# Kernel optimization log

Measured on AMD Instinct MI355X. Metric: run time of the kernel, lower is better.

Reference implementation:

```python
import jax, jax.numpy as jnp
import numpy as np

F = 16          # features
C = 128         # context features
H = 256         # conditioner hidden
L = 8           # coupling layers
K = 8           # spline bins
TB = 3.0        # tail bound
T = F // 2      # transform features per layer (8)
PDIM = 3 * K - 1  # params per transformed feature (23), tails='linear'
MIN_W = MIN_H = MIN_D = 1e-3
B = 65536


def _feature_split(layer):
    ev = np.arange(0, F, 2)
    od = np.arange(1, F, 2)
    tr, idn = (ev, od) if layer % 2 == 0 else (od, ev)  # mask>0 => transform
    inv = np.argsort(np.concatenate([idn, tr]))
    return idn, tr, inv


def _rq_spline(x, uw, uh, ud):
    """Monotonic rational-quadratic spline with linear tails (nflows semantics).
    x: [B,T]; uw/uh: [B,T,K]; ud: [B,T,K-1]. Returns (y, logabsdet) per element."""
    const = np.log(np.expm1(1.0 - MIN_D))  # pad value so boundary derivative == 1
    ud = jnp.pad(ud, ((0, 0), (0, 0), (1, 1)), constant_values=const)  # [B,T,K+1]
    inside = (x >= -TB) & (x <= TB)
    xs = jnp.clip(x, -TB, TB)

    w = jax.nn.softmax(uw, axis=-1)
    w = MIN_W + (1.0 - MIN_W * K) * w
    cw = jnp.pad(jnp.cumsum(w, -1), ((0, 0), (0, 0), (1, 0)))
    cw = 2.0 * TB * cw - TB
    cw = cw.at[..., 0].set(-TB).at[..., -1].set(TB)
    w = cw[..., 1:] - cw[..., :-1]

    d = MIN_D + jax.nn.softplus(ud)  # [B,T,K+1]

    h = jax.nn.softmax(uh, axis=-1)
    h = MIN_H + (1.0 - MIN_H * K) * h
    ch = jnp.pad(jnp.cumsum(h, -1), ((0, 0), (0, 0), (1, 0)))
    ch = 2.0 * TB * ch - TB
    ch = ch.at[..., 0].set(-TB).at[..., -1].set(TB)
    h = ch[..., 1:] - ch[..., :-1]

    # bin search on cumulative widths (forward direction)
    idx = jnp.clip(jnp.sum((xs[..., None] >= cw).astype(jnp.int32), -1) - 1, 0, K - 1)
    g = lambda a: jnp.take_along_axis(a, idx[..., None], axis=-1)[..., 0]

    x0, bw = g(cw[..., :K]), g(w)
    y0, bh = g(ch[..., :K]), g(h)
    delta = g(h / w)
    d0, d1 = g(d[..., :K]), g(d[..., 1:])

    th = (xs - x0) / bw
    th1m = th * (1.0 - th)
    num = bh * (delta * th * th + d0 * th1m)
    den = delta + (d0 + d1 - 2.0 * delta) * th1m
    y = y0 + num / den
    dnum = delta * delta * (d1 * th * th + 2.0 * delta * th1m + d0 * (1.0 - th) ** 2)
    ld = jnp.log(dnum) - 2.0 * jnp.log(den)
    return jnp.where(inside, y, x), jnp.where(inside, ld, 0.0)


def setup_inputs() -> dict:
    key = jax.random.key(0)
    ks = jax.random.split(key, 8)
    inputs = jax.random.normal(ks[0], (B, F), jnp.float32)
    context = jax.random.normal(ks[1], (B, C), jnp.float32)
    s = lambda k, shape, fan: jax.random.normal(k, shape, jnp.float32) / np.sqrt(fan)
    W1 = s(ks[2], (L, T + C, H), T + C)
    b1 = jnp.zeros((L, H), jnp.float32)
    W2 = s(ks[3], (L, H, H), H)
    b2 = jnp.zeros((L, H), jnp.float32)
    W3 = s(ks[4], (L, H, T * PDIM), H)
    b3 = jnp.zeros((L, T * PDIM), jnp.float32)
    rng = np.random.default_rng(0)  # fixed-at-init RandomPermutation buffers
    perms = jnp.asarray(np.stack([rng.permutation(F) for _ in range(L - 1)]), jnp.int32)
    return dict(inputs=inputs, context=context, W1=W1, b1=b1, W2=W2, b2=b2,
                W3=W3, b3=b3, perms=perms)


def reference(inputs, context, W1, b1, W2, b2, W3, b3, perms):
    x = jnp.clip(inputs, -1.0, 1.0)
    logdet = jnp.zeros(x.shape[0], x.dtype)
    for i in range(L):
        idn, tr, inv = _feature_split(i)
        xi = x[:, idn]
        xt = x[:, tr]
        hdn = jax.nn.relu(jnp.concatenate([xi, context], -1) @ W1[i] + b1[i])
        hdn = jax.nn.relu(hdn @ W2[i] + b2[i])
        p = (hdn @ W3[i] + b3[i]).reshape(-1, T, PDIM)
        yt, ld = _rq_spline(xt, p[..., :K], p[..., K:2 * K], p[..., 2 * K:])
        x = jnp.concatenate([xi, yt], -1)[:, inv]
        logdet = logdet + jnp.sum(ld, -1)
        if i < L - 1:
            x = x[:, perms[i]]
    return jnp.clip(x, -1.0, 1.0), logdet
```

## Files before the change

### kernel.cpp

```cpp
#include <hip/hip_runtime.h>
#include <math.h>

#define BATCH 65536
#define FDIM 16
#define CDIM 128
#define HDIM 256
#define NL 8
#define KBINS 8
#define TDIM 8
#define PD 23
#define TBV 3.0f
#define K1 160
#define N3 184
#define N3P 192
#define PSTR 197
#define MR 64
#define XSTR 40

typedef _Float16 f16;
typedef __attribute__((ext_vector_type(8))) _Float16 f16x8;
typedef __attribute__((ext_vector_type(4))) float f32x4;

__global__ __launch_bounds__(256)
void conv_w1_kernel(const float* __restrict__ W1,
                    f16* __restrict__ Wh, f16* __restrict__ Wl) {
    int idx = blockIdx.x * 256 + threadIdx.x;
    if (idx >= NL * HDIM * K1) return;
    int l = idx / (HDIM * K1);
    int rem = idx - l * (HDIM * K1);
    int n = rem / K1;
    int k = rem - n * K1;
    int row = (k < 128) ? (8 + k) : ((k < 136) ? (k - 128) : -1);
    float v = (row >= 0) ? W1[((size_t)l * 136 + row) * HDIM + n] : 0.f;
    f16 hv = (f16)v;
    Wh[idx] = hv; Wl[idx] = (f16)(v - (float)hv);
}

__global__ __launch_bounds__(256)
void conv_w2_kernel(const float* __restrict__ W2,
                    f16* __restrict__ Wh, f16* __restrict__ Wl) {
    int idx = blockIdx.x * 256 + threadIdx.x;
    if (idx >= NL * HDIM * HDIM) return;
    int l = idx / (HDIM * HDIM);
    int rem = idx - l * (HDIM * HDIM);
    int n = rem >> 8;
    int k = rem & 255;
    float v = W2[((size_t)l * HDIM + k) * HDIM + n];
    f16 hv = (f16)v;
    Wh[idx] = hv; Wl[idx] = (f16)(v - (float)hv);
}

__global__ __launch_bounds__(256)
void conv_w3_kernel(const float* __restrict__ W3,
                    f16* __restrict__ Wh, f16* __restrict__ Wl) {
    int idx = blockIdx.x * 256 + threadIdx.x;
    if (idx >= NL * N3P * HDIM) return;
    int l = idx / (N3P * HDIM);
    int rem = idx - l * (N3P * HDIM);
    int n = rem >> 8;
    int k = rem & 255;
    float v = (n < N3) ? W3[((size_t)l * HDIM + k) * N3 + n] : 0.f;
    f16 hv = (f16)v;
    Wh[idx] = hv; Wl[idx] = (f16)(v - (float)hv);
}

__global__ __launch_bounds__(256)
void conv_ctx_kernel(const float* __restrict__ ctx,
                     f16* __restrict__ ch, f16* __restrict__ cl) {
    size_t idx = ((size_t)blockIdx.x * 256 + threadIdx.x) * 4;
    if (idx >= (size_t)BATCH * CDIM) return;
    float4 v = *(const float4*)&ctx[idx];
    f16 h;
    h = (f16)v.x; ch[idx + 0] = h; cl[idx + 0] = (f16)(v.x - (float)h);
    h = (f16)v.y; ch[idx + 1] = h; cl[idx + 1] = (f16)(v.y - (float)h);
    h = (f16)v.z; ch[idx + 2] = h; cl[idx + 2] = (f16)(v.z - (float)h);
    h = (f16)v.w; ch[idx + 3] = h; cl[idx + 3] = (f16)(v.w - (float)h);
}

__device__ __forceinline__ float softplusf(float v) {
    return fmaxf(v, 0.f) + log1pf(expf(-fabsf(v)));
}

__device__ __forceinline__ void gld16(const f16* src, f16* dst) {
    __builtin_amdgcn_global_load_lds(
        (const __attribute__((address_space(1))) unsigned int*)src,
        (__attribute__((address_space(3))) unsigned int*)dst, 16, 0, 0);
}

template<int N> __device__ __forceinline__ void vmw() {
    asm volatile("s_waitcnt vmcnt(%0)" :: "n"(N) : "memory");
}
__device__ __forceinline__ void lgkmw() {
    asm volatile("s_waitcnt lgkmcnt(0)" ::: "memory");
}
__device__ __forceinline__ void barr() {
    __builtin_amdgcn_s_barrier();
    __builtin_amdgcn_sched_barrier(0);
}
__device__ __forceinline__ void lgkm_bar() {
    asm volatile("s_waitcnt lgkmcnt(0)" ::: "memory");
    __builtin_amdgcn_s_barrier();
    __builtin_amdgcn_sched_barrier(0);
}

__global__ __launch_bounds__(512, 1)
void flow_kernel(const float* __restrict__ in,
                 const f16* __restrict__ ctxh, const f16* __restrict__ ctxl,
                 const f16* __restrict__ W1h, const f16* __restrict__ W1l,
                 const f16* __restrict__ W2h, const f16* __restrict__ W2l,
                 const f16* __restrict__ W3h, const f16* __restrict__ W3l,
                 const float* __restrict__ b1, const float* __restrict__ b2,
                 const float* __restrict__ b3, const int* __restrict__ perms,
                 float* __restrict__ out) {
    __shared__ __align__(16) f16 sCtx[16384];
    __shared__ __align__(16) char warena[65536];
    __shared__ __align__(16) f16 sH[16384];
    __shared__ __align__(16) f16 sXi[2][MR * XSTR];
    __shared__ float sX[2][MR][17];
    __shared__ float sY[MR][9];
    __shared__ float sLd[MR][9];
    __shared__ float sLdet[MR];
    __shared__ float sBias[768];
    __shared__ int   sPerm[(NL - 1) * FDIM];

    float* sP = (float*)warena;

    const int tid = threadIdx.x;
    const int lane = tid & 63;
    const int w = tid >> 6;
    const int lr = lane & 15, lh = lane >> 4;
    const int bid = blockIdx.x;
    const int wgid = (bid & 7) * 32 + (bid >> 3);
    const int wcol0 = w * 32;
    const int wc3 = (w < 4) ? w * 32 : 128 + (w - 4) * 16;

    char* const wbuf = warena + w * 8192;

    auto bRd = [&](int lc) -> int {
        return lc * 64 + (((lh + (lc >> 1)) & 3) << 4);
    };

    auto stageB = [&](const f16* Wh, const f16* Wl, int b, int kt, int KD,
                      int colBase, int NC) {
        char* dst = wbuf + b * 4096;
        #pragma unroll
        for (int ii = 0; ii < 2; ++ii) {
            if (ii * 16 < NC) {
                int si = ii * 64 + lane;
                int c = si >> 2, pos = si & 3;
                int seg = (pos - (c >> 1)) & 3;
                const f16* sh = Wh + (size_t)(colBase + c) * KD + kt * 32 + seg * 8;
                const f16* sl = Wl + (size_t)(colBase + c) * KD + kt * 32 + seg * 8;
                gld16(sh, (f16*)(dst + ii * 1024 + lane * 16));
                gld16(sl, (f16*)(dst + NC * 64 + ii * 1024 + lane * 16));
            }
        }
    };

    for (int rb = 0; rb < 4; ++rb) {
        const int rbase = (rb * 256 + wgid) * MR;
        lgkm_bar();

        {
            int r = tid >> 3, c2 = (tid & 7) * 2;
            float2 v = *(const float2*)&in[(size_t)(rbase + r) * FDIM + c2];
            sX[0][r][c2 + 0] = fminf(fmaxf(v.x, -1.f), 1.f);
            sX[0][r][c2 + 1] = fminf(fmaxf(v.y, -1.f), 1.f);
        }
        if (tid < MR) sLdet[tid] = 0.f;
        if (rb == 0 && tid < (NL - 1) * FDIM) sPerm[tid] = perms[tid];

        #pragma unroll
        for (int s = 0; s < 4; ++s) {
            int slot = s * 512 + tid;
            int p = slot >> 10, sp = slot & 1023;
            int row = sp >> 4, blk = sp & 15;
            const f16* src = (p ? ctxl : ctxh)
                           + (size_t)(rbase + row) * CDIM + (blk ^ (row & 7)) * 8;
            gld16(src, &sCtx[slot * 8]);
        }

        int cur = 0;
        for (int l = 0; l < NL; ++l) {
            lgkm_bar();

            {
                float bv1 = (tid < 256) ? b1[l * HDIM + tid]
                                        : b2[l * HDIM + (tid - 256)];
                float bv3 = b3[l * N3 + (tid < N3 ? tid : N3 - 1)];
                sBias[tid] = bv1;
                if (tid < N3) sBias[512 + tid] = bv3;
            }
            if (tid < MR) {
                int r = tid, off = 1 - (l & 1);
                #pragma unroll
                for (int k = 0; k < 8; ++k) {
                    float v = sX[cur][r][2 * k + off];
                    f16 hv = (f16)v;
                    sXi[0][r * XSTR + k] = hv;
                    sXi[1][r * XSTR + k] = (f16)(v - (float)hv);
                }
                #pragma unroll
                for (int k = 8; k < 32; ++k) {
                    sXi[0][r * XSTR + k] = (f16)0.f;
                    sXi[1][r * XSTR + k] = (f16)0.f;
                }
            }
            const f16* W1hL = W1h + (size_t)l * HDIM * K1;
            const f16* W1lL = W1l + (size_t)l * HDIM * K1;
            const f16* W2hL = W2h + (size_t)l * HDIM * HDIM;
            const f16* W2lL = W2l + (size_t)l * HDIM * HDIM;
            const f16* W3hL = W3h + (size_t)l * N3P * HDIM;
            const f16* W3lL = W3l + (size_t)l * N3P * HDIM;
            stageB(W1hL, W1lL, 0, 0, K1, wcol0, 32);
            stageB(W1hL, W1lL, 1, 1, K1, wcol0, 32);
            lgkm_bar();

            f32x4 acc[4][2];
            #pragma unroll
            for (int i = 0; i < 4; ++i)
                #pragma unroll
                for (int j = 0; j < 2; ++j) acc[i][j] = (f32x4){0.f, 0.f, 0.f, 0.f};
            #pragma unroll
            for (int kt = 0; kt < 5; ++kt) {
                if (kt < 4) vmw<4>(); else vmw<0>();
                f16x8 ah[4], al[4];
                if (kt < 4) {
                    #pragma unroll
                    for (int i = 0; i < 4; ++i) {
                        int row = i * 16 + lr;
                        int byo = row * 256 + ((kt * 64 + lh * 16) ^ ((row & 7) << 4));
                        ah[i] = *(const f16x8*)((const char*)sCtx + byo);
                        al[i] = *(const f16x8*)((const char*)sCtx + 16384 + byo);
                    }
                } else {
                    #pragma unroll
                    for (int i = 0; i < 4; ++i) {
                        int row = i * 16 + lr;
                        ah[i] = *(const f16x8*)&sXi[0][row * XSTR + lh * 8];
                        al[i] = *(const f16x8*)&sXi[1][row * XSTR + lh * 8];
                    }
                }
                const char* bb = wbuf + (kt & 1) * 4096;
                __builtin_amdgcn_s_setprio(1);
                #pragma unroll
                for (int j = 0; j < 2; ++j) {
                    int cb = bRd(j * 16 + lr);
                    f16x8 bh = *(const f16x8*)(bb + cb);
                    f16x8 bl = *(const f16x8*)(bb + 2048 + cb);
                    #pragma unroll
                    for (int i = 0; i < 4; ++i) {
                        acc[i][j] = __builtin_amdgcn_mfma_f32_16x16x32_f16(ah[i], bh, acc[i][j], 0, 0, 0);
                        acc[i][j] = __builtin_amdgcn_mfma_f32_16x16x32_f16(ah[i], bl, acc[i][j], 0, 0, 0);
                        acc[i][j] = __builtin_amdgcn_mfma_f32_16x16x32_f16(al[i], bh, acc[i][j], 0, 0, 0);
                    }
                }
                __builtin_amdgcn_s_setprio(0);
                if (kt + 2 < 5) {
                    lgkmw();
                    stageB(W1hL, W1lL, kt & 1, kt + 2, K1, wcol0, 32);
                }
            }
            #pragma unroll
            for (int j = 0; j < 2; ++j) {
                int col = wcol0 + j * 16 + lr;
                float bv = sBias[col];
                #pragma unroll
                for (int i = 0; i < 4; ++i)
                    #pragma unroll
                    for (int q = 0; q < 4; ++q) {
                        float v = fmaxf(acc[i][j][q] + bv, 0.f);
                        int row = i * 16 + lh * 4 + q;
                        int e = ((row << 8) + col) ^ ((row & 7) << 3);
                        sH[e] = (f16)v;
                    }
            }
            stageB(W2hL, W2lL, 0, 0, HDIM, wcol0, 32);
            stageB(W2hL, W2lL, 1, 1, HDIM, wcol0, 32);
            lgkm_bar();

            #pragma unroll
            for (int i = 0; i < 4; ++i)
                #pragma unroll
                for (int j = 0; j < 2; ++j) acc[i][j] = (f32x4){0.f, 0.f, 0.f, 0.f};
            #pragma unroll
            for (int kt = 0; kt < 8; ++kt) {
                if (kt < 7) vmw<4>(); else vmw<0>();
                int k0 = kt * 32 + lh * 8;
                f16x8 ah[4];
                #pragma unroll
                for (int i = 0; i < 4; ++i) {
                    int row = i * 16 + lr;
                    int e = ((row << 8) + k0) ^ ((row & 7) << 3);
                    ah[i] = *(const f16x8*)&sH[e];
                }
                const char* bb = wbuf + (kt & 1) * 4096;
                __builtin_amdgcn_s_setprio(1);
                #pragma unroll
                for (int j = 0; j < 2; ++j) {
                    int cb = bRd(j * 16 + lr);
                    f16x8 bh = *(const f16x8*)(bb + cb);
                    f16x8 bl = *(const f16x8*)(bb + 2048 + cb);
                    #pragma unroll
                    for (int i = 0; i < 4; ++i) {
                        acc[i][j] = __builtin_amdgcn_mfma_f32_16x16x32_f16(ah[i], bh, acc[i][j], 0, 0, 0);
                        acc[i][j] = __builtin_amdgcn_mfma_f32_16x16x32_f16(ah[i], bl, acc[i][j], 0, 0, 0);
                    }
                }
                __builtin_amdgcn_s_setprio(0);
                if (kt + 2 < 8) {
                    lgkmw();
                    stageB(W2hL, W2lL, kt & 1, kt + 2, HDIM, wcol0, 32);
                }
            }
            barr();
            #pragma unroll
            for (int j = 0; j < 2; ++j) {
                int col = wcol0 + j * 16 + lr;
                float bv = sBias[256 + col];
                #pragma unroll
                for (int i = 0; i < 4; ++i)
                    #pragma unroll
                    for (int q = 0; q < 4; ++q) {
                        float v = fmaxf(acc[i][j][q] + bv, 0.f);
                        int row = i * 16 + lh * 4 + q;
                        int e = ((row << 8) + col) ^ ((row & 7) << 3);
                        sH[e] = (f16)v;
                    }
            }
            {
                const int NC3 = (w < 4) ? 32 : 16;
                stageB(W3hL, W3lL, 0, 0, HDIM, wc3, NC3);
                stageB(W3hL, W3lL, 1, 1, HDIM, wc3, NC3);
            }
            lgkm_bar();

            f32x4 acc3[4][2];
            #pragma unroll
            for (int i = 0; i < 4; ++i)
                #pragma unroll
                for (int j = 0; j < 2; ++j) acc3[i][j] = (f32x4){0.f, 0.f, 0.f, 0.f};
            {
                const int NC3 = (w < 4) ? 32 : 16;
                const int nc64 = NC3 * 64;
                #pragma unroll
                for (int kt = 0; kt < 8; ++kt) {
                    if (kt < 7) { if (w < 4) vmw<4>(); else vmw<2>(); }
                    else vmw<0>();
                    int k0 = kt * 32 + lh * 8;
                    f16x8 ah[4];
                    #pragma unroll
                    for (int i = 0; i < 4; ++i) {
                        int row = i * 16 + lr;
                        int e = ((row << 8) + k0) ^ ((row & 7) << 3);
                        ah[i] = *(const f16x8*)&sH[e];
                    }
                    const char* bb = wbuf + (kt & 1) * 4096;
                    __builtin_amdgcn_s_setprio(1);
                    {
                        int cb = bRd(lr);
                        f16x8 bh = *(const f16x8*)(bb + cb);
                        f16x8 bl = *(const f16x8*)(bb + nc64 + cb);
                        #pragma unroll
                        for (int i = 0; i < 4; ++i) {
                            acc3[i][0] = __builtin_amdgcn_mfma_f32_16x16x32_f16(ah[i], bh, acc3[i][0], 0, 0, 0);
                            acc3[i][0] = __builtin_amdgcn_mfma_f32_16x16x32_f16(ah[i], bl, acc3[i][0], 0, 0, 0);
                        }
                    }
                    if (w < 4) {
                        int cb = bRd(16 + lr);
                        f16x8 bh = *(const f16x8*)(bb + cb);
                        f16x8 bl = *(const f16x8*)(bb + nc64 + cb);
                        #pragma unroll
                        for (int i = 0; i < 4; ++i) {
                            acc3[i][1] = __builtin_amdgcn_mfma_f32_16x16x32_f16(ah[i], bh, acc3[i][1], 0, 0, 0);
                            acc3[i][1] = __builtin_amdgcn_mfma_f32_16x16x32_f16(ah[i], bl, acc3[i][1], 0, 0, 0);
                        }
                    }
                    __builtin_amdgcn_s_setprio(0);
                    if (kt + 2 < 8) {
                        lgkmw();
                        stageB(W3hL, W3lL, kt & 1, kt + 2, HDIM, wc3, NC3);
                    }
                }
            }
            barr();
            {
                int col = wc3 + lr;
                float bv = (col < N3) ? sBias[512 + col] : 0.f;
                #pragma unroll
                for (int i = 0; i < 4; ++i)
                    #pragma unroll
                    for (int q = 0; q < 4; ++q) {
                        int row = i * 16 + lh * 4 + q;
                        sP[row * PSTR + col] = acc3[i][0][q] + bv;
                    }
                if (w < 4) {
                    int col1 = wc3 + 16 + lr;
                    float bv1 = sBias[512 + col1];
                    #pragma unroll
                    for (int i = 0; i < 4; ++i)
                        #pragma unroll
                        for (int q = 0; q < 4; ++q) {
                            int row = i * 16 + lh * 4 + q;
                            sP[row * PSTR + col1] = acc3[i][1][q] + bv1;
                        }
                }
            }
            lgkm_bar();

            {
                int r = tid & 63, t = tid >> 6;
                float xin = sX[cur][r][2 * t + (l & 1)];
                const float* pp = &sP[r * PSTR + t * PD];
                bool inside = (xin >= -TBV) && (xin <= TBV);
                float xs = fminf(fmaxf(xin, -TBV), TBV);

                float e0, e1, e2, e3, e4, e5, e6, e7;
                {
                    float a0 = pp[0], a1 = pp[1], a2 = pp[2], a3 = pp[3];
                    float a4 = pp[4], a5 = pp[5], a6 = pp[6], a7 = pp[7];
                    float m = fmaxf(fmaxf(fmaxf(a0, a1), fmaxf(a2, a3)),
                                    fmaxf(fmaxf(a4, a5), fmaxf(a6, a7)));
                    e0 = expf(a0 - m); e1 = expf(a1 - m); e2 = expf(a2 - m); e3 = expf(a3 - m);
                    e4 = expf(a4 - m); e5 = expf(a5 - m); e6 = expf(a6 - m); e7 = expf(a7 - m);
                }
                float swv = ((e0 + e1) + (e2 + e3)) + ((e4 + e5) + (e6 + e7));
                float cwc = (1.f - 0.001f * KBINS) / swv;
                float x0 = -TBV, x1 = TBV;
                int idx = 0;
                bool done = false;
                {
                    float cs = 0.f;
                    float ee[7] = {e0, e1, e2, e3, e4, e5, e6};
                    #pragma unroll
                    for (int k = 0; k < 7; ++k) {
                        cs += 0.001f + cwc * ee[k];
                        float nxt = 2.f * TBV * cs - TBV;
                        bool ge = (xs >= nxt);
                        x0 = ge ? nxt : x0;
                        idx += ge ? 1 : 0;
                        x1 = (!ge && !done) ? nxt : x1;
                        done = done || !ge;
                    }
                }
                float y0 = -TBV, y1 = TBV;
                {
                    float a0 = pp[8], a1 = pp[9], a2 = pp[10], a3 = pp[11];
                    float a4 = pp[12], a5 = pp[13], a6 = pp[14], a7 = pp[15];
                    float m = fmaxf(fmaxf(fmaxf(a0, a1), fmaxf(a2, a3)),
                                    fmaxf(fmaxf(a4, a5), fmaxf(a6, a7)));
                    float f0 = expf(a0 - m), f1 = expf(a1 - m), f2 = expf(a2 - m), f3 = expf(a3 - m);
                    float f4 = expf(a4 - m), f5 = expf(a5 - m), f6 = expf(a6 - m), f7 = expf(a7 - m);
                    float shv = ((f0 + f1) + (f2 + f3)) + ((f4 + f5) + (f6 + f7));
                    float chc = (1.f - 0.001f * KBINS) / shv;
                    float cs = 0.f;
                    float ff[7] = {f0, f1, f2, f3, f4, f5, f6};
                    #pragma unroll
                    for (int k = 0; k < 7; ++k) {
                        cs += 0.001f + chc * ff[k];
                        float nxt = 2.f * TBV * cs - TBV;
                        y0 = (k < idx) ? nxt : y0;
                        y1 = (k == idx) ? nxt : y1;
                    }
                }
                float udm = pp[16 + (idx > 0 ? idx - 1 : 0)];
                float udp = pp[16 + (idx < 7 ? idx : 6)];
                float d0 = (idx > 0) ? 0.001f + softplusf(udm) : 1.f;
                float d1 = (idx < 7) ? 0.001f + softplusf(udp) : 1.f;

                float bw = x1 - x0, bh2 = y1 - y0;
                float delta = bh2 / bw;
                float th = (xs - x0) / bw;
                float th1m = th * (1.f - th);
                float num = bh2 * (delta * th * th + d0 * th1m);
                float den = delta + (d0 + d1 - 2.f * delta) * th1m;
                float y = y0 + num / den;
                float omth = 1.f - th;
                float dnum = delta * delta * (d1 * th * th + 2.f * delta * th1m + d0 * omth * omth);
                float ldv = logf(dnum) - 2.f * logf(den);
                sY[r][t] = inside ? y : xin;
                sLd[r][t] = inside ? ldv : 0.f;
            }
            lgkm_bar();

            {
                int r = tid >> 3, f0 = (tid & 7) * 2;
                if (l < NL - 1) {
                    #pragma unroll
                    for (int ff = 0; ff < 2; ++ff) {
                        int f = f0 + ff;
                        int g = sPerm[l * FDIM + f];
                        float v = ((g & 1) == (l & 1)) ? sY[r][g >> 1] : sX[cur][r][g];
                        sX[cur ^ 1][r][f] = v;
                    }
                    if (f0 == 0) {
                        float s = 0.f;
                        #pragma unroll
                        for (int t = 0; t < 8; ++t) s += sLd[r][t];
                        sLdet[r] += s;
                    }
                } else {
                    float ov[2];
                    #pragma unroll
                    for (int ff = 0; ff < 2; ++ff) {
                        int f = f0 + ff;
                        float v = ((f & 1) == (l & 1)) ? sY[r][f >> 1] : sX[cur][r][f];
                        ov[ff] = fminf(fmaxf(v, -1.f), 1.f);
                    }
                    float2 o = {ov[0], ov[1]};
                    *(float2*)&out[(size_t)(rbase + r) * FDIM + f0] = o;
                    if (f0 == 0) {
                        float s = 0.f;
                        #pragma unroll
                        for (int t = 0; t < 8; ++t) s += sLd[r][t];
                        out[(size_t)BATCH * FDIM + rbase + r] = sLdet[r] + s;
                    }
                }
            }
            cur ^= 1;
        }
    }
}

extern "C" void kernel_launch(void* const* d_in, const int* in_sizes, int n_in,
                              void* d_out, int out_size, void* d_ws, size_t ws_size,
                              hipStream_t stream) {
    (void)in_sizes; (void)n_in; (void)out_size; (void)ws_size;
    const float* inputs  = (const float*)d_in[0];
    const float* context = (const float*)d_in[1];
    const float* W1 = (const float*)d_in[2];
    const float* b1 = (const float*)d_in[3];
    const float* W2 = (const float*)d_in[4];
    const float* b2 = (const float*)d_in[5];
    const float* W3 = (const float*)d_in[6];
    const float* b3 = (const float*)d_in[7];
    const int*   perms = (const int*)d_in[8];
    float* out = (float*)d_out;

    f16* W1h = (f16*)d_ws;
    f16* W1l = W1h + (size_t)NL * HDIM * K1;
    f16* W2h = W1l + (size_t)NL * HDIM * K1;
    f16* W2l = W2h + (size_t)NL * HDIM * HDIM;
    f16* W3h = W2l + (size_t)NL * HDIM * HDIM;
    f16* W3l = W3h + (size_t)NL * N3P * HDIM;
    f16* ctxh = W3l + (size_t)NL * N3P * HDIM;
    f16* ctxl = ctxh + (size_t)BATCH * CDIM;

    int n1 = NL * HDIM * K1;
    conv_w1_kernel<<<(n1 + 255) / 256, 256, 0, stream>>>(W1, W1h, W1l);
    int n2 = NL * HDIM * HDIM;
    conv_w2_kernel<<<(n2 + 255) / 256, 256, 0, stream>>>(W2, W2h, W2l);
    int n3 = NL * N3P * HDIM;
    conv_w3_kernel<<<(n3 + 255) / 256, 256, 0, stream>>>(W3, W3h, W3l);
    int nc = BATCH * CDIM / 4;
    conv_ctx_kernel<<<(nc + 255) / 256, 256, 0, stream>>>(context, ctxh, ctxl);

    flow_kernel<<<256, 512, 0, stream>>>(
        inputs, ctxh, ctxl, W1h, W1l, W2h, W2l, W3h, W3l,
        b1, b2, b3, perms, out);
}
```

Measured before the change: 520.4 us.

## Split hidden activations into hi/lo f16 and keep W2/W3 single f16

Moves the fp16 hi/lo error-compensation split from the W2/W3 weights to the hidden activations. Weights are now converted to a single f16 copy, which halves weight staging traffic and the per-wave LDS weight buffers. The low part of each activation is stored in a new shared region carved out of the weight arena. The MFMA count stays the same, but W2/W3 weights lose their low-order correction, which may reduce accuracy. An extra barrier is added after layer 1, presumably because the activation low part now shares LDS with the weight staging buffers.

```diff
diff --git a/kernel.cpp b/kernel.cpp
--- a/kernel.cpp
+++ b/kernel.cpp
@@ -37,22 +37,18 @@
 }
 
 __global__ __launch_bounds__(256)
-void conv_w2_kernel(const float* __restrict__ W2,
-                    f16* __restrict__ Wh, f16* __restrict__ Wl) {
+void conv_w2_kernel(const float* __restrict__ W2, f16* __restrict__ Ws) {
     int idx = blockIdx.x * 256 + threadIdx.x;
     if (idx >= NL * HDIM * HDIM) return;
     int l = idx / (HDIM * HDIM);
     int rem = idx - l * (HDIM * HDIM);
     int n = rem >> 8;
     int k = rem & 255;
-    float v = W2[((size_t)l * HDIM + k) * HDIM + n];
-    f16 hv = (f16)v;
-    Wh[idx] = hv; Wl[idx] = (f16)(v - (float)hv);
+    Ws[idx] = (f16)W2[((size_t)l * HDIM + k) * HDIM + n];
 }
 
 __global__ __launch_bounds__(256)
-void conv_w3_kernel(const float* __restrict__ W3,
-                    f16* __restrict__ Wh, f16* __restrict__ Wl) {
+void conv_w3_kernel(const float* __restrict__ W3, f16* __restrict__ Ws) {
     int idx = blockIdx.x * 256 + threadIdx.x;
     if (idx >= NL * N3P * HDIM) return;
     int l = idx / (N3P * HDIM);
@@ -60,8 +56,7 @@
     int n = rem >> 8;
     int k = rem & 255;
     float v = (n < N3) ? W3[((size_t)l * HDIM + k) * N3 + n] : 0.f;
-    f16 hv = (f16)v;
-    Wh[idx] = hv; Wl[idx] = (f16)(v - (float)hv);
+    Ws[idx] = (f16)v;
 }
 
 __global__ __launch_bounds__(256)
@@ -107,8 +102,7 @@
 void flow_kernel(const float* __restrict__ in,
                  const f16* __restrict__ ctxh, const f16* __restrict__ ctxl,
                  const f16* __restrict__ W1h, const f16* __restrict__ W1l,
-                 const f16* __restrict__ W2h, const f16* __restrict__ W2l,
-                 const f16* __restrict__ W3h, const f16* __restrict__ W3l,
+                 const f16* __restrict__ W2s, const f16* __restrict__ W3s,
                  const float* __restrict__ b1, const float* __restrict__ b2,
                  const float* __restrict__ b3, const int* __restrict__ perms,
                  float* __restrict__ out) {
@@ -123,6 +117,7 @@
     __shared__ float sBias[768];
     __shared__ int   sPerm[(NL - 1) * FDIM];
 
+    f16* hLo = (f16*)(warena + 32768);
     float* sP = (float*)warena;
 
     const int tid = threadIdx.x;
@@ -134,28 +129,23 @@
     const int wcol0 = w * 32;
     const int wc3 = (w < 4) ? w * 32 : 128 + (w - 4) * 16;
 
-    char* const wbuf = warena + w * 8192;
-
     auto bRd = [&](int lc) -> int {
         return lc * 64 + (((lh + (lc >> 1)) & 3) << 4);
     };
 
-    auto stageB = [&](const f16* Wh, const f16* Wl, int b, int kt, int KD,
-                      int colBase, int NC) {
-        char* dst = wbuf + b * 4096;
+    auto stageB1 = [&](int b, int kt) {
+        char* dst = warena + w * 8192 + b * 4096;
+        const f16* WhL = W1h;
+        (void)WhL;
         #pragma unroll
         for (int ii = 0; ii < 2; ++ii) {
-            if (ii * 16 < NC) {
-                int si = ii * 64 + lane;
-                int c = si >> 2, pos = si & 3;
-                int seg = (pos - (c >> 1)) & 3;
-                const f16* sh = Wh + (size_t)(colBase + c) * KD + kt * 32 + seg * 8;
-                const f16* sl = Wl + (size_t)(colBase + c) * KD + kt * 32 + seg * 8;
-                gld16(sh, (f16*)(dst + ii * 1024 + lane * 16));
-                gld16(sl, (f16*)(dst + NC * 64 + ii * 1024 + lane * 16));
-            }
+            int si = ii * 64 + lane;
+            int c = si >> 2, pos = si & 3;
+            int seg = (pos - (c >> 1)) & 3;
+            (void)c; (void)seg; (void)dst; (void)kt;
         }
     };
+    (void)stageB1;
 
     for (int rb = 0; rb < 4; ++rb) {
         const int rbase = (rb * 256 + wgid) * MR;
@@ -202,18 +192,44 @@
                 }
                 #pragma unroll
                 for (int k = 8; k < 32; ++k) {
-                    sXi[0][r * XSTR + k] = (f16)0.f;
-                    sXi[1][r * XSTR + k] = (f16)0.f;
+                    sXi[0][tid * XSTR + k] = (f16)0.f;
+                    sXi[1][tid * XSTR + k] = (f16)0.f;
                 }
             }
             const f16* W1hL = W1h + (size_t)l * HDIM * K1;
             const f16* W1lL = W1l + (size_t)l * HDIM * K1;
-            const f16* W2hL = W2h + (size_t)l * HDIM * HDIM;
-            const f16* W2lL = W2l + (size_t)l * HDIM * HDIM;
-            const f16* W3hL = W3h + (size_t)l * N3P * HDIM;
-            const f16* W3lL = W3l + (size_t)l * N3P * HDIM;
-            stageB(W1hL, W1lL, 0, 0, K1, wcol0, 32);
-            stageB(W1hL, W1lL, 1, 1, K1, wcol0, 32);
+            const f16* W2L  = W2s + (size_t)l * HDIM * HDIM;
+            const f16* W3L  = W3s + (size_t)l * N3P * HDIM;
+
+            auto stage1 = [&](int b, int kt) {
+                char* dst = warena + w * 8192 + b * 4096;
+                #pragma unroll
+                for (int ii = 0; ii < 2; ++ii) {
+                    int si = ii * 64 + lane;
+                    int c = si >> 2, pos = si & 3;
+                    int seg = (pos - (c >> 1)) & 3;
+                    const f16* sh = W1hL + (size_t)(wcol0 + c) * K1 + kt * 32 + seg * 8;
+                    const f16* sl = W1lL + (size_t)(wcol0 + c) * K1 + kt * 32 + seg * 8;
+                    gld16(sh, (f16*)(dst + ii * 1024 + lane * 16));
+                    gld16(sl, (f16*)(dst + 2048 + ii * 1024 + lane * 16));
+                }
+            };
+            auto stageS = [&](const f16* W, int b, int kt, int colBase, int NC) {
+                char* dst = warena + w * 4096 + b * 2048;
+                #pragma unroll
+                for (int ii = 0; ii < 2; ++ii) {
+                    if (ii * 16 < NC) {
+                        int si = ii * 64 + lane;
+                        int c = si >> 2, pos = si & 3;
+                        int seg = (pos - (c >> 1)) & 3;
+                        gld16(W + (size_t)(colBase + c) * HDIM + kt * 32 + seg * 8,
+                              (f16*)(dst + ii * 1024 + lane * 16));
+                    }
+                }
+            };
+
+            stage1(0, 0);
+            stage1(1, 1);
             lgkm_bar();
 
             f32x4 acc[4][2];
@@ -241,7 +257,7 @@
                         al[i] = *(const f16x8*)&sXi[1][row * XSTR + lh * 8];
                     }
                 }
-                const char* bb = wbuf + (kt & 1) * 4096;
+                const char* bb = warena + w * 8192 + (kt & 1) * 4096;
                 __builtin_amdgcn_s_setprio(1);
                 #pragma unroll
                 for (int j = 0; j < 2; ++j) {
@@ -258,9 +274,10 @@
                 __builtin_amdgcn_s_setprio(0);
                 if (kt + 2 < 5) {
                     lgkmw();
-                    stageB(W1hL, W1lL, kt & 1, kt + 2, K1, wcol0, 32);
-                }
-            }
+                    stage1(kt & 1, kt + 2);
+                }
+            }
+            barr();
             #pragma unroll
             for (int j = 0; j < 2; ++j) {
                 int col = wcol0 + j * 16 + lr;
@@ -272,11 +289,13 @@
                         float v = fmaxf(acc[i][j][q] + bv, 0.f);
                         int row = i * 16 + lh * 4 + q;
                         int e = ((row << 8) + col) ^ ((row & 7) << 3);
-                        sH[e] = (f16)v;
-                    }
-            }
-            stageB(W2hL, W2lL, 0, 0, HDIM, wcol0, 32);
-            stageB(W2hL, W2lL, 1, 1, HDIM, wcol0, 32);
+                        f16 hv = (f16)v;
+                        sH[e] = hv;
+                        hLo[e] = (f16)(v - (float)hv);
+                    }
+            }
+            stageS(W2L, 0, 0, wcol0, 32);
+            stageS(W2L, 1, 1, wcol0, 32);
             lgkm_bar();
 
             #pragma unroll
@@ -285,32 +304,32 @@
                 for (int j = 0; j < 2; ++j) acc[i][j] = (f32x4){0.f, 0.f, 0.f, 0.f};
             #pragma unroll
             for (int kt = 0; kt < 8; ++kt) {
-                if (kt < 7) vmw<4>(); else vmw<0>();
+                if (kt < 7) vmw<2>(); else vmw<0>();
                 int k0 = kt * 32 + lh * 8;
-                f16x8 ah[4];
+                f16x8 ah[4], al[4];
                 #pragma unroll
                 for (int i = 0; i < 4; ++i) {
                     int row = i * 16 + lr;
                     int e = ((row << 8) + k0) ^ ((row & 7) << 3);
                     ah[i] = *(const f16x8*)&sH[e];
-                }
-                const char* bb = wbuf + (kt & 1) * 4096;
+                    al[i] = *(const f16x8*)&hLo[e];
+                }
+                const char* bb = warena + w * 4096 + (kt & 1) * 2048;
                 __builtin_amdgcn_s_setprio(1);
                 #pragma unroll
                 for (int j = 0; j < 2; ++j) {
                     int cb = bRd(j * 16 + lr);
-                    f16x8 bh = *(const f16x8*)(bb + cb);
-                    f16x8 bl = *(const f16x8*)(bb + 2048 + cb);
+                    f16x8 b = *(const f16x8*)(bb + cb);
                     #pragma unroll
                     for (int i = 0; i < 4; ++i) {
-                        acc[i][j] = __builtin_amdgcn_mfma_f32_16x16x32_f16(ah[i], bh, acc[i][j], 0, 0, 0);
-                        acc[i][j] = __builtin_amdgcn_mfma_f32_16x16x32_f16(ah[i], bl, acc[i][j], 0, 0, 0);
+                        acc[i][j] = __builtin_amdgcn_mfma_f32_16x16x32_f16(ah[i], b, acc[i][j], 0, 0, 0);
+                        acc[i][j] = __builtin_amdgcn_mfma_f32_16x16x32_f16(al[i], b, acc[i][j], 0, 0, 0);
                     }
                 }
                 __builtin_amdgcn_s_setprio(0);
                 if (kt + 2 < 8) {
                     lgkmw();
-                    stageB(W2hL, W2lL, kt & 1, kt + 2, HDIM, wcol0, 32);
+                    stageS(W2L, kt & 1, kt + 2, wcol0, 32);
                 }
             }
             barr();
@@ -325,13 +344,15 @@
                         float v = fmaxf(acc[i][j][q] + bv, 0.f);
                         int row = i * 16 + lh * 4 + q;
                         int e = ((row << 8) + col) ^ ((row & 7) << 3);
-                        sH[e] = (f16)v;
+                        f16 hv = (f16)v;
+                        sH[e] = hv;
+                        hLo[e] = (f16)(v - (float)hv);
                     }
             }
             {
                 const int NC3 = (w < 4) ? 32 : 16;
-                stageB(W3hL, W3lL, 0, 0, HDIM, wc3, NC3);
-                stageB(W3hL, W3lL, 1, 1, HDIM, wc3, NC3);
+                stageS(W3L, 0, 0, wc3, NC3);
+                stageS(W3L, 1, 1, wc3, NC3);
             }
             lgkm_bar();
 
@@ -342,45 +363,43 @@
                 for (int j = 0; j < 2; ++j) acc3[i][j] = (f32x4){0.f, 0.f, 0.f, 0.f};
             {
                 const int NC3 = (w < 4) ? 32 : 16;
-                const int nc64 = NC3 * 64;
                 #pragma unroll
                 for (int kt = 0; kt < 8; ++kt) {
-                    if (kt < 7) { if (w < 4) vmw<4>(); else vmw<2>(); }
+                    if (kt < 7) { if (w < 4) vmw<2>(); else vmw<1>(); }
                     else vmw<0>();
                     int k0 = kt * 32 + lh * 8;
-                    f16x8 ah[4];
+                    f16x8 ah[4], al[4];
                     #pragma unroll
                     for (int i = 0; i < 4; ++i) {
                         int row = i * 16 + lr;
                         int e = ((row << 8) + k0) ^ ((row & 7) << 3);
                         ah[i] = *(const f16x8*)&sH[e];
-                    }
-                    const char* bb = wbuf + (kt & 1) * 4096;
+                        al[i] = *(const f16x8*)&hLo[e];
+                    }
+                    const char* bb = warena + w * 4096 + (kt & 1) * 2048;
                     __builtin_amdgcn_s_setprio(1);
                     {
                         int cb = bRd(lr);
-                        f16x8 bh = *(const f16x8*)(bb + cb);
-                        f16x8 bl = *(const f16x8*)(bb + nc64 + cb);
+                        f16x8 b = *(const f16x8*)(bb + cb);
                         #pragma unroll
                         for (int i = 0; i < 4; ++i) {
-                            acc3[i][0] = __builtin_amdgcn_mfma_f32_16x16x32_f16(ah[i], bh, acc3[i][0], 0, 0, 0);
-                            acc3[i][0] = __builtin_amdgcn_mfma_f32_16x16x32_f16(ah[i], bl, acc3[i][0], 0, 0, 0);
+                            acc3[i][0] = __builtin_amdgcn_mfma_f32_16x16x32_f16(ah[i], b, acc3[i][0], 0, 0, 0);
+                            acc3[i][0] = __builtin_amdgcn_mfma_f32_16x16x32_f16(al[i], b, acc3[i][0], 0, 0, 0);
                         }
                     }
                     if (w < 4) {
                         int cb = bRd(16 + lr);
-                        f16x8 bh = *(const f16x8*)(bb + cb);
-                        f16x8 bl = *(const f16x8*)(bb + nc64 + cb);
+                        f16x8 b = *(const f16x8*)(bb + cb);
                         #pragma unroll
                         for (int i = 0; i < 4; ++i) {
-                            acc3[i][1] = __builtin_amdgcn_mfma_f32_16x16x32_f16(ah[i], bh, acc3[i][1], 0, 0, 0);
-                            acc3[i][1] = __builtin_amdgcn_mfma_f32_16x16x32_f16(ah[i], bl, acc3[i][1], 0, 0, 0);
+                            acc3[i][1] = __builtin_amdgcn_mfma_f32_16x16x32_f16(ah[i], b, acc3[i][1], 0, 0, 0);
+                            acc3[i][1] = __builtin_amdgcn_mfma_f32_16x16x32_f16(al[i], b, acc3[i][1], 0, 0, 0);
                         }
                     }
                     __builtin_amdgcn_s_setprio(0);
                     if (kt + 2 < 8) {
                         lgkmw();
-                        stageB(W3hL, W3lL, kt & 1, kt + 2, HDIM, wc3, NC3);
+                        stageS(W3L, kt & 1, kt + 2, wc3, NC3);
                     }
                 }
             }
@@ -540,23 +559,21 @@
 
     f16* W1h = (f16*)d_ws;
     f16* W1l = W1h + (size_t)NL * HDIM * K1;
-    f16* W2h = W1l + (size_t)NL * HDIM * K1;
-    f16* W2l = W2h + (size_t)NL * HDIM * HDIM;
-    f16* W3h = W2l + (size_t)NL * HDIM * HDIM;
-    f16* W3l = W3h + (size_t)NL * N3P * HDIM;
-    f16* ctxh = W3l + (size_t)NL * N3P * HDIM;
+    f16* W2sp = W1l + (size_t)NL * HDIM * K1;
+    f16* W3sp = W2sp + (size_t)NL * HDIM * HDIM;
+    f16* ctxh = W3sp + (size_t)NL * N3P * HDIM;
     f16* ctxl = ctxh + (size_t)BATCH * CDIM;
 
     int n1 = NL * HDIM * K1;
     conv_w1_kernel<<<(n1 + 255) / 256, 256, 0, stream>>>(W1, W1h, W1l);
     int n2 = NL * HDIM * HDIM;
-    conv_w2_kernel<<<(n2 + 255) / 256, 256, 0, stream>>>(W2, W2h, W2l);
+    conv_w2_kernel<<<(n2 + 255) / 256, 256, 0, stream>>>(W2, W2sp);
     int n3 = NL * N3P * HDIM;
-    conv_w3_kernel<<<(n3 + 255) / 256, 256, 0, stream>>>(W3, W3h, W3l);
+    conv_w3_kernel<<<(n3 + 255) / 256, 256, 0, stream>>>(W3, W3sp);
     int nc = BATCH * CDIM / 4;
     conv_ctx_kernel<<<(nc + 255) / 256, 256, 0, stream>>>(context, ctxh, ctxl);
 
     flow_kernel<<<256, 512, 0, stream>>>(
-        inputs, ctxh, ctxl, W1h, W1l, W2h, W2l, W3h, W3l,
+        inputs, ctxh, ctxl, W1h, W1l, W2sp, W3sp,
         b1, b2, b3, perms, out);
 }
```

Result: slower. 618.1 us (+18.8%).
